# Optimization experiments

Measured on AMD Instinct MI355X. Metric: run time of the kernel, lower is better.

## Reference

```python
import jax, jax.numpy as jnp
import numpy as np

DIM = 256
N_EMBED = 4096


def setup_inputs() -> dict:
    key = jax.random.key(0)
    k1, k2 = jax.random.split(key)
    x = jax.random.normal(k1, (16, 4096, DIM), dtype=jnp.float32)
    embed = jax.random.normal(k2, (DIM, N_EMBED), dtype=jnp.float32)  # codebook buffer [dim, n_embed]
    return {"x": x, "embed": embed}


def reference(x, embed):
    # Eval-mode VQ forward (OT=False): cdist -> argmin -> gather -> straight-through.
    dim = embed.shape[0]
    flatten = x.reshape(-1, dim)  # [N, dim]
    # Squared L2 distance to every codebook entry: [N, n_embed]
    dist = (
        jnp.sum(flatten * flatten, axis=1, keepdims=True)
        - 2.0 * (flatten @ embed)
        + jnp.sum(embed * embed, axis=0, keepdims=True)
    )
    embed_ind_flat = jnp.argmax(-dist, axis=1)  # nearest code per token
    embed_ind = embed_ind_flat.reshape(x.shape[:-1])
    # one-hot embedding lookup == gather rows of embed.T
    quantize = jnp.take(embed.T, embed_ind_flat, axis=0).reshape(x.shape)
    diff = jnp.mean((jax.lax.stop_gradient(quantize) - x) ** 2)
    quantize = x + jax.lax.stop_gradient(quantize - x)  # straight-through estimator
    return (quantize, diff, embed_ind)
```

## Files before the change

kernel.cpp:

```cpp
#include <hip/hip_runtime.h>

typedef unsigned int u32;

#define N_TOK 65536
#define DIM 256
#define NE 4096
#define TM 128
#define TN 256
#define TK 32
#define NET (NE / TN)

__device__ __align__(16) float g_enorm[NE];
__device__ __align__(16) float g_xnorm[N_TOK];
__device__ float g_diffarr[64];

__device__ __forceinline__ float sqr_rn(float v) { return __fmul_rn(v, v); }

__device__ __forceinline__ void load16_lds(const float* __restrict__ g, float* l) {
    __builtin_amdgcn_global_load_lds(
        (const __attribute__((address_space(1))) void*)g,
        (__attribute__((address_space(3))) void*)l, 16, 0, 0);
}

__device__ float np_sum128_sq(const float* __restrict__ a) {
    float r[8];
#pragma unroll
    for (int j = 0; j < 8; ++j) r[j] = sqr_rn(a[j]);
    for (int i = 8; i < 128; i += 8)
#pragma unroll
        for (int j = 0; j < 8; ++j) r[j] = __fadd_rn(r[j], sqr_rn(a[i + j]));
    return __fadd_rn(__fadd_rn(__fadd_rn(r[0], r[1]), __fadd_rn(r[2], r[3])),
                     __fadd_rn(__fadd_rn(r[4], r[5]), __fadd_rn(r[6], r[7])));
}

__global__ void k_xnorm(const float* __restrict__ x) {
    const int n = blockIdx.x * 256 + threadIdx.x;
    const float* row = x + (size_t)n * DIM;
    g_xnorm[n] = __fadd_rn(np_sum128_sq(row), np_sum128_sq(row + 128));
    if (blockIdx.x == 0 && threadIdx.x < 64) g_diffarr[threadIdx.x] = 0.f;
}

__global__ void k_enorm(const float* __restrict__ embed) {
    const int e = blockIdx.x * 256 + threadIdx.x;
    float s = sqr_rn(embed[e]);
    for (int d = 1; d < DIM; ++d) s = __fadd_rn(s, sqr_rn(embed[(size_t)d * NE + e]));
    g_enorm[e] = s;
}

__global__ __launch_bounds__(512, 2)
void k_argmin(const float* __restrict__ x, const float* __restrict__ embed,
              float* __restrict__ out_ind) {
    __shared__ __align__(16) float xs[TM * TK];
    __shared__ __align__(16) float es[TK * TN];
    const int tid = threadIdx.x;
    const int tx = tid & 31;
    const int ty = tid >> 5;
    const int n0 = blockIdx.x * TM;

    float best[8];
    int bidx[8];
#pragma unroll
    for (int i = 0; i < 8; i++) { best[i] = 3.0e38f; bidx[i] = 0; }

#pragma unroll 1
    for (int et = 0; et < NET; ++et) {
        const int e0 = et * TN;
        float acc[8][8];
#pragma unroll
        for (int i = 0; i < 8; i++)
#pragma unroll
            for (int j = 0; j < 8; j++) acc[i][j] = 0.f;

#pragma unroll 1
        for (int kt = 0; kt < DIM / TK; ++kt) {
            const int k0 = kt * TK;
            __syncthreads();
#pragma unroll
            for (int i_ = 0; i_ < 2; ++i_) {
                const int f_ = i_ * 512 + tid;
                const int r_ = f_ >> 3, c_ = f_ & 7;
                load16_lds(x + (size_t)(n0 + r_) * DIM + k0 + c_ * 4, xs + f_ * 4);
            }
#pragma unroll
            for (int i_ = 0; i_ < 4; ++i_) {
                const int f_ = i_ * 512 + tid;
                const int r_ = f_ >> 6, c_ = f_ & 63;
                load16_lds(embed + (size_t)(k0 + r_) * NE + e0 + c_ * 4, es + f_ * 4);
            }
            __syncthreads();

#pragma unroll 1
            for (int g = 0; g < 8; ++g) {
                float4 ea[4], eb[4];
#pragma unroll
                for (int kk = 0; kk < 4; ++kk) {
                    const int kb = (g * 4 + kk) * TN;
                    ea[kk] = *(const float4*)&es[kb + tx * 4];
                    eb[kk] = *(const float4*)&es[kb + 128 + tx * 4];
                }
#pragma unroll
                for (int i = 0; i < 8; ++i) {
                    const float4 xt = *(const float4*)&xs[(i * 16 + ty) * TK + g * 4];
#pragma unroll
                    for (int kk = 0; kk < 4; ++kk) {
                        const float xk = kk == 0 ? xt.x
                                       : kk == 1 ? xt.y
                                       : kk == 2 ? xt.z : xt.w;
                        acc[i][0] = fmaf(xk, ea[kk].x, acc[i][0]);
                        acc[i][1] = fmaf(xk, ea[kk].y, acc[i][1]);
                        acc[i][2] = fmaf(xk, ea[kk].z, acc[i][2]);
                        acc[i][3] = fmaf(xk, ea[kk].w, acc[i][3]);
                        acc[i][4] = fmaf(xk, eb[kk].x, acc[i][4]);
                        acc[i][5] = fmaf(xk, eb[kk].y, acc[i][5]);
                        acc[i][6] = fmaf(xk, eb[kk].z, acc[i][6]);
                        acc[i][7] = fmaf(xk, eb[kk].w, acc[i][7]);
                    }
                }
            }
        }

        const float4 ena = *(const float4*)&g_enorm[e0 + tx * 4];
        const float4 enb = *(const float4*)&g_enorm[e0 + 128 + tx * 4];
        const float enj[8] = {ena.x, ena.y, ena.z, ena.w, enb.x, enb.y, enb.z, enb.w};
#pragma unroll
        for (int i = 0; i < 8; i++) {
            const float xnv = g_xnorm[n0 + i * 16 + ty];
#pragma unroll
            for (int j = 0; j < 8; j++) {
                float v = __fadd_rn(__fsub_rn(xnv, __fmul_rn(2.0f, acc[i][j])), enj[j]);
                int e = e0 + (j >> 2) * 128 + tx * 4 + (j & 3);
                if (v < best[i]) { best[i] = v; bidx[i] = e; }
            }
        }
    }
#pragma unroll
    for (int i = 0; i < 8; i++) {
        float b = best[i];
        int bi = bidx[i];
#pragma unroll
        for (int m = 1; m < 32; m <<= 1) {
            float ob = __shfl_xor(b, m, 64);
            int oi = __shfl_xor(bi, m, 64);
            if (ob < b || (ob == b && oi < bi)) { b = ob; bi = oi; }
        }
        if (tx == 0) out_ind[n0 + i * 16 + ty] = (float)bi;
    }
}

__global__ void k_gather(const float* __restrict__ x, const float* __restrict__ embed,
                         const float* __restrict__ out_ind, float* __restrict__ outq) {
    const int n = blockIdx.x;
    const int d = threadIdx.x;
    int e = (int)out_ind[n];
    e = e < 0 ? 0 : (e > NE - 1 ? NE - 1 : e);
    const float v = embed[(size_t)d * NE + e];
    outq[(size_t)n * DIM + d] = v;
    float sq = v - x[(size_t)n * DIM + d];
    sq *= sq;
#pragma unroll
    for (int m = 1; m < 64; m <<= 1) sq += __shfl_xor(sq, m, 64);
    __shared__ float wsum[4];
    if ((d & 63) == 0) wsum[d >> 6] = sq;
    __syncthreads();
    if (d == 0) atomicAdd(&g_diffarr[n & 63], wsum[0] + wsum[1] + wsum[2] + wsum[3]);
}

__global__ void k_finish(float* __restrict__ out_diff) {
    float t = 0.f;
    for (int w = 0; w < 64; ++w) t += g_diffarr[w];
    if (threadIdx.x == 0) *out_diff = t * (1.0f / 16777216.0f);
}

extern "C" void kernel_launch(void* const* d_in, const int* in_sizes, int n_in,
                              void* d_out, int out_size, void* d_ws, size_t ws_size,
                              hipStream_t stream) {
    const float* x = (const float*)d_in[0];
    const float* embed = (const float*)d_in[1];
    float* outq = (float*)d_out;
    float* out_diff = outq + 16777216;
    float* out_ind = outq + 16777217;

    hipLaunchKernelGGL(k_xnorm, dim3(N_TOK / 256), dim3(256), 0, stream, x);
    hipLaunchKernelGGL(k_enorm, dim3(NE / 256), dim3(256), 0, stream, embed);
    hipLaunchKernelGGL(k_argmin, dim3(N_TOK / TM), dim3(512), 0, stream, x, embed, out_ind);
    hipLaunchKernelGGL(k_gather, dim3(N_TOK), dim3(256), 0, stream, x, embed, out_ind, outq);
    hipLaunchKernelGGL(k_finish, dim3(1), dim3(64), 0, stream, out_diff);
}
```

Measured before the change: 2.011 ms.

## Double-buffer LDS tiles in argmin GEMM to overlap loads with compute

The argmin kernel's nested e-tile/k-tile loops are flattened into one loop with ping-pong LDS buffers for both x and embed. The next tile's global-to-LDS loads are issued right after the barrier, so they overlap the FMA work on the current tile, and one barrier per step is removed. The cost is twice the LDS per block (96KB). That likely caps residency at one 512-thread block per CU instead of two, giving up some latency hiding from occupancy.

```diff
diff --git a/kernel.cpp b/kernel.cpp
--- a/kernel.cpp
+++ b/kernel.cpp
@@ -9,6 +9,7 @@
 #define TN 256
 #define TK 32
 #define NET (NE / TN)
+#define NT (NET * 8)
 
 __device__ __align__(16) float g_enorm[NE];
 __device__ __align__(16) float g_xnorm[N_TOK];
@@ -50,86 +51,101 @@
 __global__ __launch_bounds__(512, 2)
 void k_argmin(const float* __restrict__ x, const float* __restrict__ embed,
               float* __restrict__ out_ind) {
-    __shared__ __align__(16) float xs[TM * TK];
-    __shared__ __align__(16) float es[TK * TN];
+    __shared__ __align__(16) float xs0[TM * TK];
+    __shared__ __align__(16) float xs1[TM * TK];
+    __shared__ __align__(16) float es0[TK * TN];
+    __shared__ __align__(16) float es1[TK * TN];
     const int tid = threadIdx.x;
     const int tx = tid & 31;
     const int ty = tid >> 5;
     const int n0 = blockIdx.x * TM;
 
+    auto stage = [&](float* xsd, float* esd, int t) {
+        const int k0 = (t & 7) * TK;
+        const int e0_ = (t >> 3) * TN;
+#pragma unroll
+        for (int i_ = 0; i_ < 2; ++i_) {
+            const int f_ = i_ * 512 + tid;
+            const int r_ = f_ >> 3, c_ = f_ & 7;
+            load16_lds(x + (size_t)(n0 + r_) * DIM + k0 + c_ * 4, xsd + f_ * 4);
+        }
+#pragma unroll
+        for (int i_ = 0; i_ < 4; ++i_) {
+            const int f_ = i_ * 512 + tid;
+            const int r_ = f_ >> 6, c_ = f_ & 63;
+            load16_lds(embed + (size_t)(k0 + r_) * NE + e0_ + c_ * 4, esd + f_ * 4);
+        }
+    };
+
+    stage(xs0, es0, 0);
+
     float best[8];
     int bidx[8];
 #pragma unroll
     for (int i = 0; i < 8; i++) { best[i] = 3.0e38f; bidx[i] = 0; }
 
+    float acc[8][8];
 #pragma unroll 1
-    for (int et = 0; et < NET; ++et) {
-        const int e0 = et * TN;
-        float acc[8][8];
-#pragma unroll
-        for (int i = 0; i < 8; i++)
-#pragma unroll
-            for (int j = 0; j < 8; j++) acc[i][j] = 0.f;
+    for (int t = 0; t < NT; ++t) {
+        const int kt = t & 7;
+        if (kt == 0) {
+#pragma unroll
+            for (int i = 0; i < 8; i++)
+#pragma unroll
+                for (int j = 0; j < 8; j++) acc[i][j] = 0.f;
+        }
+        __syncthreads();
+        if (t + 1 < NT) {
+            if (t & 1) stage(xs0, es0, t + 1);
+            else       stage(xs1, es1, t + 1);
+        }
+        const float* __restrict__ xsr = (t & 1) ? xs1 : xs0;
+        const float* __restrict__ esr = (t & 1) ? es1 : es0;
 
 #pragma unroll 1
-        for (int kt = 0; kt < DIM / TK; ++kt) {
-            const int k0 = kt * TK;
-            __syncthreads();
-#pragma unroll
-            for (int i_ = 0; i_ < 2; ++i_) {
-                const int f_ = i_ * 512 + tid;
-                const int r_ = f_ >> 3, c_ = f_ & 7;
-                load16_lds(x + (size_t)(n0 + r_) * DIM + k0 + c_ * 4, xs + f_ * 4);
+        for (int g = 0; g < 8; ++g) {
+            float4 ea[4], eb[4];
+#pragma unroll
+            for (int kk = 0; kk < 4; ++kk) {
+                const int kb = (g * 4 + kk) * TN;
+                ea[kk] = *(const float4*)&esr[kb + tx * 4];
+                eb[kk] = *(const float4*)&esr[kb + 128 + tx * 4];
             }
 #pragma unroll
-            for (int i_ = 0; i_ < 4; ++i_) {
-                const int f_ = i_ * 512 + tid;
-                const int r_ = f_ >> 6, c_ = f_ & 63;
-                load16_lds(embed + (size_t)(k0 + r_) * NE + e0 + c_ * 4, es + f_ * 4);
-            }
-            __syncthreads();
-
-#pragma unroll 1
-            for (int g = 0; g < 8; ++g) {
-                float4 ea[4], eb[4];
+            for (int i = 0; i < 8; ++i) {
+                const float4 xt = *(const float4*)&xsr[(i * 16 + ty) * TK + g * 4];
 #pragma unroll
                 for (int kk = 0; kk < 4; ++kk) {
-                    const int kb = (g * 4 + kk) * TN;
-                    ea[kk] = *(const float4*)&es[kb + tx * 4];
-                    eb[kk] = *(const float4*)&es[kb + 128 + tx * 4];
-                }
-#pragma unroll
-                for (int i = 0; i < 8; ++i) {
-                    const float4 xt = *(const float4*)&xs[(i * 16 + ty) * TK + g * 4];
-#pragma unroll
-                    for (int kk = 0; kk < 4; ++kk) {
-                        const float xk = kk == 0 ? xt.x
-                                       : kk == 1 ? xt.y
-                                       : kk == 2 ? xt.z : xt.w;
-                        acc[i][0] = fmaf(xk, ea[kk].x, acc[i][0]);
-                        acc[i][1] = fmaf(xk, ea[kk].y, acc[i][1]);
-                        acc[i][2] = fmaf(xk, ea[kk].z, acc[i][2]);
-                        acc[i][3] = fmaf(xk, ea[kk].w, acc[i][3]);
-                        acc[i][4] = fmaf(xk, eb[kk].x, acc[i][4]);
-                        acc[i][5] = fmaf(xk, eb[kk].y, acc[i][5]);
-                        acc[i][6] = fmaf(xk, eb[kk].z, acc[i][6]);
-                        acc[i][7] = fmaf(xk, eb[kk].w, acc[i][7]);
-                    }
+                    const float xk = kk == 0 ? xt.x
+                                   : kk == 1 ? xt.y
+                                   : kk == 2 ? xt.z : xt.w;
+                    acc[i][0] = fmaf(xk, ea[kk].x, acc[i][0]);
+                    acc[i][1] = fmaf(xk, ea[kk].y, acc[i][1]);
+                    acc[i][2] = fmaf(xk, ea[kk].z, acc[i][2]);
+                    acc[i][3] = fmaf(xk, ea[kk].w, acc[i][3]);
+                    acc[i][4] = fmaf(xk, eb[kk].x, acc[i][4]);
+                    acc[i][5] = fmaf(xk, eb[kk].y, acc[i][5]);
+                    acc[i][6] = fmaf(xk, eb[kk].z, acc[i][6]);
+                    acc[i][7] = fmaf(xk, eb[kk].w, acc[i][7]);
                 }
             }
         }
 
-        const float4 ena = *(const float4*)&g_enorm[e0 + tx * 4];
-        const float4 enb = *(const float4*)&g_enorm[e0 + 128 + tx * 4];
-        const float enj[8] = {ena.x, ena.y, ena.z, ena.w, enb.x, enb.y, enb.z, enb.w};
-#pragma unroll
-        for (int i = 0; i < 8; i++) {
-            const float xnv = g_xnorm[n0 + i * 16 + ty];
-#pragma unroll
-            for (int j = 0; j < 8; j++) {
-                float v = __fadd_rn(__fsub_rn(xnv, __fmul_rn(2.0f, acc[i][j])), enj[j]);
-                int e = e0 + (j >> 2) * 128 + tx * 4 + (j & 3);
-                if (v < best[i]) { best[i] = v; bidx[i] = e; }
+        if (kt == 7) {
+            const int e0 = (t >> 3) * TN;
+            const float4 ena = *(const float4*)&g_enorm[e0 + tx * 4];
+            const float4 enb = *(const float4*)&g_enorm[e0 + 128 + tx * 4];
+            const float enj[8] = {ena.x, ena.y, ena.z, ena.w,
+                                  enb.x, enb.y, enb.z, enb.w};
+#pragma unroll
+            for (int i = 0; i < 8; i++) {
+                const float xnv = g_xnorm[n0 + i * 16 + ty];
+#pragma unroll
+                for (int j = 0; j < 8; j++) {
+                    float v = __fadd_rn(__fsub_rn(xnv, __fmul_rn(2.0f, acc[i][j])), enj[j]);
+                    int e = e0 + (j >> 2) * 128 + tx * 4 + (j & 3);
+                    if (v < best[i]) { best[i] = v; bidx[i] = e; }
+                }
             }
         }
     }
```

Measured after the change: 1.995 ms. About the same (-0.8%).
